# Kernel optimization log

Hardware: AMD Instinct MI355X
Metric: run time of the kernel (lower is better)

Reference implementation:

```python
import jax, jax.numpy as jnp
import numpy as np

KH = KW = 3
K = KH * KW
STRIDE = 1
PAD = 1
DIL = 1
GROUPS = 1
DG = 1  # deformable_groups
CIN = 256
COUT = 256
DC = 64  # depth_channels


def conv2d(x, w, b):
    out = jax.lax.conv_general_dilated(
        x, w, (STRIDE, STRIDE), [(PAD, PAD), (PAD, PAD)],
        rhs_dilation=(DIL, DIL), dimension_numbers=('NCHW', 'OIHW', 'NCHW'))
    return out + b[None, :, None, None]


def deform_sample(x, offset, mask):
    """Modulated deformable im2col. x:[N,C,H,W], offset:[N,DG*2*K,Ho,Wo],
    mask:[N,DG*K,Ho,Wo] or None. Returns cols [N,C,K,Ho,Wo]."""
    N, C, H, W = x.shape
    Ho = (H + 2 * PAD - (DIL * (KH - 1) + 1)) // STRIDE + 1
    Wo = (W + 2 * PAD - (DIL * (KW - 1) + 1)) // STRIDE + 1
    ky, kx = jnp.meshgrid(jnp.arange(KH), jnp.arange(KW), indexing='ij')
    # base sampling grid per kernel tap: [K,Ho,Wo]
    base_y = (jnp.arange(Ho) * STRIDE - PAD)[None, :, None] + (ky.reshape(-1) * DIL)[:, None, None]
    base_x = (jnp.arange(Wo) * STRIDE - PAD)[None, None, :] + (kx.reshape(-1) * DIL)[:, None, None]
    off = offset.reshape(N, DG, K, 2, Ho, Wo)  # [...,0]=dy, [...,1]=dx (CUDA layout)
    y = base_y[None, None].astype(x.dtype) + off[:, :, :, 0]
    xx = base_x[None, None].astype(x.dtype) + off[:, :, :, 1]
    y0 = jnp.floor(y)
    x0 = jnp.floor(xx)
    ly = y - y0
    lx = xx - x0
    y0i = y0.astype(jnp.int32)
    x0i = x0.astype(jnp.int32)
    xg = x.reshape(N, DG, C // DG, H * W)

    def gather(iy, ix):
        valid = ((iy >= 0) & (iy < H) & (ix >= 0) & (ix < W)).astype(x.dtype)
        idx = (jnp.clip(iy, 0, H - 1) * W + jnp.clip(ix, 0, W - 1)).reshape(N, DG, 1, K * Ho * Wo)
        v = jnp.take_along_axis(xg, idx, axis=3).reshape(N, DG, C // DG, K, Ho, Wo)
        return v * valid[:, :, None]

    v00 = gather(y0i, x0i)
    v01 = gather(y0i, x0i + 1)
    v10 = gather(y0i + 1, x0i)
    v11 = gather(y0i + 1, x0i + 1)
    w00 = (1 - ly) * (1 - lx)
    w01 = (1 - ly) * lx
    w10 = ly * (1 - lx)
    w11 = ly * lx
    cols = (v00 * w00[:, :, None] + v01 * w01[:, :, None]
            + v10 * w10[:, :, None] + v11 * w11[:, :, None])
    if mask is not None:
        cols = cols * mask.reshape(N, DG, 1, K, Ho, Wo)
    return cols.reshape(N, C, K, Ho, Wo)


def deform_conv2d(x, offset, mask, weight, bias):
    cols = deform_sample(x, offset, mask)  # [N,C,K,Ho,Wo]
    N, C, _, Ho, Wo = cols.shape
    Cout = weight.shape[0]
    cg = C // GROUPS
    cols = cols.reshape(N, GROUPS, cg * K, Ho * Wo)
    wg = weight.reshape(GROUPS, Cout // GROUPS, cg * K)
    out = jnp.einsum('gok,ngkp->ngop', wg, cols).reshape(N, Cout, Ho, Wo)
    return out + bias[None, :, None, None]


def setup_inputs() -> dict:
    key = jax.random.key(0)
    ks = jax.random.split(key, 8)
    x = jax.random.normal(ks[0], (4, CIN, 64, 64), dtype=jnp.float32)
    depth = jax.random.normal(ks[1], (4, DC, 64, 64), dtype=jnp.float32)
    stdv = 1.0 / np.sqrt(CIN * KH * KW)
    weight = jax.random.uniform(ks[2], (COUT, CIN // GROUPS, KH, KW), minval=-stdv, maxval=stdv, dtype=jnp.float32)
    bias = jnp.zeros((COUT,), jnp.float32)
    # offset/mask convs are zero-init in the module; use small random weights
    # so the irregular gather path is actually exercised.
    off_w = 0.05 * jax.random.normal(ks[3], (DG * 2 * K, CIN + DC, KH, KW), dtype=jnp.float32)
    off_b = 0.05 * jax.random.normal(ks[4], (DG * 2 * K,), dtype=jnp.float32)
    mask_w = 0.05 * jax.random.normal(ks[5], (DG * K, DC, KH, KW), dtype=jnp.float32)
    mask_b = 0.05 * jax.random.normal(ks[6], (DG * K,), dtype=jnp.float32)
    return {"x": x, "depth": depth, "weight": weight, "bias": bias,
            "off_w": off_w, "off_b": off_b, "mask_w": mask_w, "mask_b": mask_b}


def reference(x, depth, weight, bias, off_w, off_b, mask_w, mask_b):
    # offset = conv_offset(cat(x, depth))
    offset = conv2d(jnp.concatenate([x, depth], axis=1), off_w, off_b)
    # mask = sigmoid(DeformConv(depth, offset))  (non-modulated deform conv)
    mask = jax.nn.sigmoid(deform_conv2d(depth, offset, None, mask_w, mask_b))
    # modulated deformable conv on x
    return deform_conv2d(x, offset, mask, weight, bias)
```

## Files before the change

kernel.cpp:

```cpp
#include <hip/hip_runtime.h>


typedef __bf16 bf16x8 __attribute__((ext_vector_type(8)));
typedef float f32x4 __attribute__((ext_vector_type(4)));
typedef float float2_u __attribute__((ext_vector_type(2), aligned(4)));

__device__ __forceinline__ unsigned short f2bf(float f) {
  unsigned b = __float_as_uint(f);
  return (unsigned short)((b + 0x7fffu + ((b >> 16) & 1u)) >> 16);
}

__global__ __launch_bounds__(256) void k_prep_weight(
    const float* __restrict__ w, unsigned short* __restrict__ wbf)
{
  const int i = blockIdx.x * 256 + threadIdx.x;
  wbf[i] = f2bf(w[i]);
}

__global__ __launch_bounds__(256) void k_offset_conv(
    const float* __restrict__ x, const float* __restrict__ depth,
    const float* __restrict__ off_w, const float* __restrict__ off_b,
    float* __restrict__ offs)
{
  const int seg = blockIdx.x >> 8;
  const int nh  = blockIdx.x & 255;
  const int n = nh >> 6, ho = nh & 63;
  const int tid = threadIdx.x;
  const int lane = tid & 63;
  const int wave = tid >> 6;

  float acc[18];
#pragma unroll
  for (int i = 0; i < 18; ++i) acc[i] = 0.f;

  const int c0 = __builtin_amdgcn_readfirstlane(seg * 80 + wave * 20);

  for (int ci = 0; ci < 20; ++ci) {
    const int c = c0 + ci;
    const float* p = (c < 256) ? (x + (((n << 8) + c) << 12))
                               : (depth + (((n << 6) + (c - 256)) << 12));
    const float v0 = (ho > 0)  ? p[((ho - 1) << 6) + lane] : 0.f;
    const float v1 =             p[( ho      << 6) + lane];
    const float v2 = (ho < 63) ? p[((ho + 1) << 6) + lane] : 0.f;

    float v[9];
#pragma unroll
    for (int ky = 0; ky < 3; ++ky) {
      const float r = (ky == 0) ? v0 : ((ky == 1) ? v1 : v2);
#pragma unroll
      for (int kx = 0; kx < 3; ++kx) {
        const int src = lane + kx - 1;
        const float s = __shfl(r, src & 63);
        v[ky * 3 + kx] = (src >= 0 && src < 64) ? s : 0.f;
      }
    }
    const float* wp = off_w + c * 9;
#pragma unroll
    for (int co = 0; co < 18; ++co) {
      const float* w = wp + co * 2880;
#pragma unroll
      for (int t = 0; t < 9; ++t) acc[co] += v[t] * w[t];
    }
  }

  __shared__ float red[4][18][64];
#pragma unroll
  for (int co = 0; co < 18; ++co) red[wave][co][lane] = acc[co];
  __syncthreads();
  for (int o = tid; o < 18 * 64; o += 256) {
    const int co = o >> 6, wo = o & 63;
    float s = red[0][co][wo] + red[1][co][wo] + red[2][co][wo] + red[3][co][wo];
    if (seg == 0) s += off_b[co];
    atomicAdd(&offs[((n * 18 + co) << 12) + (ho << 6) + wo], s);
  }
}

__global__ __launch_bounds__(512) void k_mask_conv(
    const float* __restrict__ depth, const float* __restrict__ offs,
    const float* __restrict__ mask_w, const float* __restrict__ mask_b,
    float* __restrict__ mask)
{
  const int n  = blockIdx.x >> 6;
  const int ho = blockIdx.x & 63;
  const int tid  = threadIdx.x;
  const int lane = tid & 63;
  const int wave = tid >> 6;
  const int wo = lane;

  int i00[9], i01[9], i10[9], i11[9];
  float cw00[9], cw01[9], cw10[9], cw11[9];
  const float* op = offs + ((n * 18) << 12) + (ho << 6) + wo;
#pragma unroll
  for (int k = 0; k < 9; ++k) {
    const float dy = op[(2 * k) << 12];
    const float dx = op[(2 * k + 1) << 12];
    const float yy = (float)(ho - 1 + k / 3) + dy;
    const float xx = (float)(wo - 1 + k % 3) + dx;
    const float y0f = floorf(yy), x0f = floorf(xx);
    const float ly = yy - y0f, lx = xx - x0f;
    const int y0 = (int)y0f, x0 = (int)x0f;
    const int y0c = min(max(y0, 0), 63),     x0c = min(max(x0, 0), 63);
    const int y1c = min(max(y0 + 1, 0), 63), x1c = min(max(x0 + 1, 0), 63);
    const float fy0 = (y0 >= 0 && y0 < 64) ? 1.f : 0.f;
    const float fy1 = (y0 >= -1 && y0 < 63) ? 1.f : 0.f;
    const float fx0 = (x0 >= 0 && x0 < 64) ? 1.f : 0.f;
    const float fx1 = (x0 >= -1 && x0 < 63) ? 1.f : 0.f;
    i00[k] = (y0c << 6) + x0c;  i01[k] = (y0c << 6) + x1c;
    i10[k] = (y1c << 6) + x0c;  i11[k] = (y1c << 6) + x1c;
    cw00[k] = (1.f - ly) * (1.f - lx) * fy0 * fx0;
    cw01[k] = (1.f - ly) * lx * fy0 * fx1;
    cw10[k] = ly * (1.f - lx) * fy1 * fx0;
    cw11[k] = ly * lx * fy1 * fx1;
  }

  float acc[9];
#pragma unroll
  for (int i = 0; i < 9; ++i) acc[i] = 0.f;

  const int cbase = __builtin_amdgcn_readfirstlane(wave * 8);
  for (int cc = 0; cc < 8; ++cc) {
    const int c = cbase + cc;
    const float* p = depth + (((n << 6) + c) << 12);
    float val[9];
#pragma unroll
    for (int k = 0; k < 9; ++k) {
      val[k] = p[i00[k]] * cw00[k] + p[i01[k]] * cw01[k] +
               p[i10[k]] * cw10[k] + p[i11[k]] * cw11[k];
    }
    const float* wp = mask_w + c * 9;
#pragma unroll
    for (int co = 0; co < 9; ++co) {
#pragma unroll
      for (int k = 0; k < 9; ++k) acc[co] += val[k] * wp[co * 576 + k];
    }
  }

  __shared__ float red[8][9][64];
#pragma unroll
  for (int co = 0; co < 9; ++co) red[wave][co][lane] = acc[co];
  __syncthreads();
  for (int o = tid; o < 9 * 64; o += 512) {
    const int co = o >> 6, w2 = o & 63;
    float s = mask_b[co];
#pragma unroll
    for (int w = 0; w < 8; ++w) s += red[w][co][w2];
    mask[((n * 9 + co) << 12) + (ho << 6) + w2] = 1.f / (1.f + expf(-s));
  }
}

__device__ __forceinline__ void stage_channel8k(const float* src, float* dstb,
                                                int lane) {
  const char* s = (const char*)src + lane * 16;
  char* d = (char*)dstb;
#pragma unroll
  for (int j = 0; j < 8; ++j)
    __builtin_amdgcn_global_load_lds(
        (const __attribute__((address_space(1))) void*)(s + j * 1024),
        (__attribute__((address_space(3))) void*)(d + j * 1024), 16, 0, 0);
}

__global__ __launch_bounds__(512, 2) void k_deform_gemm(
    const float* __restrict__ x, const float* __restrict__ offs,
    const float* __restrict__ mask, const unsigned short* __restrict__ wbf,
    const float* __restrict__ bias, float* __restrict__ out)
{
  __shared__ float strip[9 * 2048];
  __shared__ __align__(16) unsigned short Bs[64][72];
  __shared__ float4 pwT[9][64];
  __shared__ int    piT[9][64];
  __shared__ int    piF[9][64];

  const int tid = threadIdx.x;
  const int b    = blockIdx.x;
  const int xcd  = b & 7, bslot = b >> 3;
  const int n    = xcd >> 1;
  const int ho   = ((xcd & 1) << 5) + bslot;
  const int pxb  = ho << 6;
  const int ylo  = min(max(ho - 15, 0), 32);

  for (int e = tid; e < 576; e += 512) {
    const int tap = e >> 6, pl = e & 63;
    const int wo = pl;
    const float dy = offs[((n * 18 + 2 * tap) << 12) + pxb + pl];
    const float dx = offs[((n * 18 + 2 * tap + 1) << 12) + pxb + pl];
    const float m  = mask[((n * 9 + tap) << 12) + pxb + pl];
    const float yy = (float)(ho - 1 + tap / 3) + dy;
    const float xx = (float)(wo - 1 + tap % 3) + dx;
    const float y0f = floorf(yy), x0f = floorf(xx);
    const float ly = yy - y0f, lx = xx - x0f;
    const int y0 = (int)y0f, x0 = (int)x0f;
    const int y0c = min(max(y0, 0), 63);
    const int y1c = min(max(y0 + 1, 0), 63);
    const float fy0 = (y0 >= 0 && y0 < 64) ? 1.f : 0.f;
    const float fy1 = (y0 >= -1 && y0 < 63) ? 1.f : 0.f;
    const int x0c = min(max(x0, 0), 63);
    const int x1c = min(max(x0 + 1, 0), 63);
    const int bx  = min(max(x0, 0), 62);
    const float vx0 = (x0 >= 0 && x0 < 64) ? 1.f : 0.f;
    const float vx1 = (x0 >= -1 && x0 < 63) ? 1.f : 0.f;
    const float wl = (1.f - lx) * vx0 * ((x0c == bx) ? 1.f : 0.f)
                   + lx * vx1 * ((x1c == bx) ? 1.f : 0.f);
    const float wr = (1.f - lx) * vx0 * ((x0c == bx + 1) ? 1.f : 0.f)
                   + lx * vx1 * ((x1c == bx + 1) ? 1.f : 0.f);
    const float a0 = (1.f - ly) * fy0 * m;
    const float a1 = ly * fy1 * m;
    pwT[tap][pl] = make_float4(wl * a0, wr * a0, wl * a1, wr * a1);
    const int ry0 = y0c - ylo, ry1 = y1c - ylo;
    const int ry0c = min(max(ry0, 0), 31), ry1c = min(max(ry1, 0), 31);
    const int bad = ((ry0 != ry0c) || (ry1 != ry1c)) ? 1 : 0;
    const int ad0 = (ry0c << 8) | (bx << 2);
    const int ad1 = (ry1c << 8) | (bx << 2);
    piT[tap][pl] = ad0 | (ad1 << 13) | (bad << 26);
    piF[tap][pl] = bx | (y0c << 6) | (y1c << 12);
  }

  const int pxl  = tid & 63;
  const int oct  = tid >> 6;
  const int lane = tid & 63;
  const int mrow = lane & 15;
  const int koct = lane >> 4;
  const float* xn = x + ((long)(n << 8) << 12);
  const char* xnc = (const char*)xn;
  const char* stripb = (const char*)strip;

  stage_channel8k(xn + (oct << 12) + (ylo << 6), &strip[oct * 2048], lane);
  int c_staged = 8;
  __syncthreads();

  auto gather = [&](int ic) {
    const int k0 = (ic << 6) + (oct << 3);
    int tp[8], sof[8];
#pragma unroll
    for (int j = 0; j < 8; ++j) {
      const int k = k0 + j;
      const int c = (int)(((unsigned)k * 7282u) >> 16);
      tp[j] = k - 9 * c;
      const int s9 = (int)(((unsigned)c * 7282u) >> 16);
      sof[j] = (c - 9 * s9) << 13;
    }
    int pk[8];
#pragma unroll
    for (int j = 0; j < 8; ++j) pk[j] = piT[tp[j]][pxl];
    float4 w[8];
#pragma unroll
    for (int j = 0; j < 8; ++j) w[j] = pwT[tp[j]][pxl];
    float2_u A[8], B[8];
#pragma unroll
    for (int j = 0; j < 8; ++j) {
      A[j] = *(const float2_u*)(stripb + sof[j] + (pk[j] & 8191));
      B[j] = *(const float2_u*)(stripb + sof[j] + ((pk[j] >> 13) & 8191));
    }
    int badm = 0;
    __align__(16) unsigned short v[8];
#pragma unroll
    for (int j = 0; j < 8; ++j) {
      v[j] = f2bf(A[j].x * w[j].x + A[j].y * w[j].y +
                  B[j].x * w[j].z + B[j].y * w[j].w);
      badm |= (pk[j] >> 26) << j;
    }
    if (__builtin_expect(badm != 0, 0)) {
#pragma unroll
      for (int j = 0; j < 8; ++j) if (badm & (1 << j)) {
        const int k = k0 + j;
        const int c = (int)(((unsigned)k * 7282u) >> 16);
        const char* pg = xnc + ((long)c << 14);
        const int pf = piF[tp[j]][pxl];
        const int bx = pf & 63, y0c = (pf >> 6) & 63, y1c = (pf >> 12) & 63;
        const float2_u Ag = *(const float2_u*)(pg + ((((y0c << 6) + bx)) << 2));
        const float2_u Bg = *(const float2_u*)(pg + ((((y1c << 6) + bx)) << 2));
        v[j] = f2bf(Ag.x * w[j].x + Ag.y * w[j].y +
                    Bg.x * w[j].z + Bg.y * w[j].w);
      }
    }
    *(int4*)&Bs[pxl][oct << 3] = *(const int4*)v;
  };

  bf16x8 afc[2][2];
#pragma unroll
  for (int mt = 0; mt < 2; ++mt)
#pragma unroll
    for (int ks = 0; ks < 2; ++ks) {
      const int row = (oct << 5) + (mt << 4) + mrow;
      const int col = (ks << 5) + (koct << 3);
      afc[mt][ks] = *(const bf16x8*)(wbf + row * 2304 + col);
    }

  gather(0);
  __syncthreads();

  f32x4 acc[2][4];
#pragma unroll
  for (int mt = 0; mt < 2; ++mt)
#pragma unroll
    for (int nt = 0; nt < 4; ++nt)
#pragma unroll
      for (int r = 0; r < 4; ++r) acc[mt][nt][r] = 0.f;

  for (int ic = 0; ic < 36; ++ic) {
    if (ic < 35) {
      const int c_end = (64 * ic + 127) / 9;
      const int cw = c_staged + oct;
      if (cw <= c_end) {
        const int slt = cw - 9 * (int)(((unsigned)cw * 7282u) >> 16);
        stage_channel8k(xn + (cw << 12) + (ylo << 6), &strip[slt * 2048], lane);
      }
      c_staged = c_end + 1;
    }

    bf16x8 afn[2][2];
    if (ic < 35) {
      const int kc = (ic + 1) << 6;
#pragma unroll
      for (int mt = 0; mt < 2; ++mt)
#pragma unroll
        for (int ks = 0; ks < 2; ++ks) {
          const int row = (oct << 5) + (mt << 4) + mrow;
          const int col = kc + (ks << 5) + (koct << 3);
          afn[mt][ks] = *(const bf16x8*)(wbf + row * 2304 + col);
        }
    }

#pragma unroll
    for (int ks = 0; ks < 2; ++ks)
#pragma unroll
      for (int nt = 0; nt < 4; ++nt) {
        const bf16x8 bfr =
            *(const bf16x8*)&Bs[(nt << 4) + mrow][(ks << 5) + (koct << 3)];
        acc[0][nt] = __builtin_amdgcn_mfma_f32_16x16x32_bf16(afc[0][ks], bfr,
                                                             acc[0][nt], 0, 0, 0);
        acc[1][nt] = __builtin_amdgcn_mfma_f32_16x16x32_bf16(afc[1][ks], bfr,
                                                             acc[1][nt], 0, 0, 0);
      }

    __syncthreads();
    if (ic < 35) gather(ic + 1);
    __syncthreads();

#pragma unroll
    for (int mt = 0; mt < 2; ++mt)
#pragma unroll
      for (int ks = 0; ks < 2; ++ks) afc[mt][ks] = afn[mt][ks];
  }

#pragma unroll
  for (int mt = 0; mt < 2; ++mt)
#pragma unroll
    for (int nt = 0; nt < 4; ++nt)
#pragma unroll
      for (int r = 0; r < 4; ++r) {
        const int co = (oct << 5) + (mt << 4) + ((lane >> 4) << 2) + r;
        const int pxg = pxb + (nt << 4) + (lane & 15);
        out[(((n << 8) + co) << 12) + pxg] = acc[mt][nt][r] + bias[co];
      }
}

extern "C" void kernel_launch(void* const* d_in, const int* in_sizes, int n_in,
                              void* d_out, int out_size, void* d_ws, size_t ws_size,
                              hipStream_t stream) {
  const float* x      = (const float*)d_in[0];
  const float* depth  = (const float*)d_in[1];
  const float* weight = (const float*)d_in[2];
  const float* bias   = (const float*)d_in[3];
  const float* off_w  = (const float*)d_in[4];
  const float* off_b  = (const float*)d_in[5];
  const float* mask_w = (const float*)d_in[6];
  const float* mask_b = (const float*)d_in[7];
  float* out = (float*)d_out;

  float* offs = (float*)d_ws;
  float* mask = offs + 294912;
  unsigned short* wbf = (unsigned short*)(mask + 147456);

  hipMemsetAsync(offs, 0, 294912 * sizeof(float), stream);
  k_prep_weight<<<2304, 256, 0, stream>>>(weight, wbf);
  k_offset_conv<<<1024, 256, 0, stream>>>(x, depth, off_w, off_b, offs);
  k_mask_conv<<<256, 512, 0, stream>>>(depth, offs, mask_w, mask_b, mask);
  k_deform_gemm<<<256, 512, 0, stream>>>(x, offs, mask, wbf, bias, out);
}
```

Measured before the change: 264.2 us.

## Keep sampling params in registers, pad LDS strip rows, stage via registers

Per-tap bilinear weights and packed addresses move from shared-memory tables into per-thread registers. The gather loop is specialised at compile time on the starting tap via a switch, and the strip base offsets become wave-uniform scalars. The input strip rows are padded to 272 bytes to cut LDS bank conflicts on the gather reads. Staging switches from global_load_lds to register loads written to LDS after the MFMA block. The rare out-of-strip fallback now recomputes its offsets from global memory, which costs more registers and risks lower occupancy.

```diff
diff --git a/kernel.cpp b/kernel.cpp
--- a/kernel.cpp
+++ b/kernel.cpp
@@ -4,6 +4,8 @@
 typedef __bf16 bf16x8 __attribute__((ext_vector_type(8)));
 typedef float f32x4 __attribute__((ext_vector_type(4)));
 typedef float float2_u __attribute__((ext_vector_type(2), aligned(4)));
+
+template <int N> struct IC { static constexpr int v = N; };
 
 __device__ __forceinline__ unsigned short f2bf(float f) {
   unsigned b = __float_as_uint(f);
@@ -148,27 +150,13 @@
   }
 }
 
-__device__ __forceinline__ void stage_channel8k(const float* src, float* dstb,
-                                                int lane) {
-  const char* s = (const char*)src + lane * 16;
-  char* d = (char*)dstb;
-#pragma unroll
-  for (int j = 0; j < 8; ++j)
-    __builtin_amdgcn_global_load_lds(
-        (const __attribute__((address_space(1))) void*)(s + j * 1024),
-        (__attribute__((address_space(3))) void*)(d + j * 1024), 16, 0, 0);
-}
-
 __global__ __launch_bounds__(512, 2) void k_deform_gemm(
     const float* __restrict__ x, const float* __restrict__ offs,
     const float* __restrict__ mask, const unsigned short* __restrict__ wbf,
     const float* __restrict__ bias, float* __restrict__ out)
 {
-  __shared__ float strip[9 * 2048];
+  __shared__ float strip[9 * 2176];
   __shared__ __align__(16) unsigned short Bs[64][72];
-  __shared__ float4 pwT[9][64];
-  __shared__ int    piT[9][64];
-  __shared__ int    piF[9][64];
 
   const int tid = threadIdx.x;
   const int b    = blockIdx.x;
@@ -178,12 +166,31 @@
   const int pxb  = ho << 6;
   const int ylo  = min(max(ho - 15, 0), 32);
 
-  for (int e = tid; e < 576; e += 512) {
-    const int tap = e >> 6, pl = e & 63;
-    const int wo = pl;
-    const float dy = offs[((n * 18 + 2 * tap) << 12) + pxb + pl];
-    const float dx = offs[((n * 18 + 2 * tap + 1) << 12) + pxb + pl];
-    const float m  = mask[((n * 9 + tap) << 12) + pxb + pl];
+  const int pxl  = tid & 63;
+  const int oct  = tid >> 6;
+  const int lane = tid & 63;
+  const int mrow = lane & 15;
+  const int koct = lane >> 4;
+  const float* xn = x + ((long)(n << 8) << 12);
+  const char* xnc = (const char*)xn;
+  const char* stripc = (const char*)strip;
+
+  float4 stg[8];
+  {
+    const char* src = (const char*)(xn + (oct << 12) + (ylo << 6)) + lane * 16;
+#pragma unroll
+    for (int i = 0; i < 8; ++i)
+      stg[i] = *(const float4*)(src + i * 1024);
+  }
+
+  float4 pw_[9];
+  int    pi_[9];
+#pragma unroll
+  for (int tap = 0; tap < 9; ++tap) {
+    const int wo = pxl;
+    const float dy = offs[((n * 18 + 2 * tap) << 12) + pxb + pxl];
+    const float dx = offs[((n * 18 + 2 * tap + 1) << 12) + pxb + pxl];
+    const float m  = mask[((n * 9 + tap) << 12) + pxb + pxl];
     const float yy = (float)(ho - 1 + tap / 3) + dy;
     const float xx = (float)(wo - 1 + tap % 3) + dx;
     const float y0f = floorf(yy), x0f = floorf(xx);
@@ -204,72 +211,93 @@
                    + lx * vx1 * ((x1c == bx + 1) ? 1.f : 0.f);
     const float a0 = (1.f - ly) * fy0 * m;
     const float a1 = ly * fy1 * m;
-    pwT[tap][pl] = make_float4(wl * a0, wr * a0, wl * a1, wr * a1);
+    pw_[tap] = make_float4(wl * a0, wr * a0, wl * a1, wr * a1);
     const int ry0 = y0c - ylo, ry1 = y1c - ylo;
     const int ry0c = min(max(ry0, 0), 31), ry1c = min(max(ry1, 0), 31);
     const int bad = ((ry0 != ry0c) || (ry1 != ry1c)) ? 1 : 0;
-    const int ad0 = (ry0c << 8) | (bx << 2);
-    const int ad1 = (ry1c << 8) | (bx << 2);
-    piT[tap][pl] = ad0 | (ad1 << 13) | (bad << 26);
-    piF[tap][pl] = bx | (y0c << 6) | (y1c << 12);
-  }
-
-  const int pxl  = tid & 63;
-  const int oct  = tid >> 6;
-  const int lane = tid & 63;
-  const int mrow = lane & 15;
-  const int koct = lane >> 4;
-  const float* xn = x + ((long)(n << 8) << 12);
-  const char* xnc = (const char*)xn;
-  const char* stripb = (const char*)strip;
-
-  stage_channel8k(xn + (oct << 12) + (ylo << 6), &strip[oct * 2048], lane);
+    const int ad0 = ry0c * 272 + (bx << 2);
+    const int ad1 = ry1c * 272 + (bx << 2);
+    pi_[tap] = ad0 | (ad1 << 14) | (bad << 28);
+  }
+
+  {
+    char* dst = (char*)strip + oct * 8704 + (lane >> 4) * 272 + (lane & 15) * 16;
+#pragma unroll
+    for (int i = 0; i < 8; ++i)
+      *(float4*)(dst + i * 4 * 272) = stg[i];
+  }
   int c_staged = 8;
   __syncthreads();
 
   auto gather = [&](int ic) {
     const int k0 = (ic << 6) + (oct << 3);
-    int tp[8], sof[8];
-#pragma unroll
-    for (int j = 0; j < 8; ++j) {
-      const int k = k0 + j;
-      const int c = (int)(((unsigned)k * 7282u) >> 16);
-      tp[j] = k - 9 * c;
-      const int s9 = (int)(((unsigned)c * 7282u) >> 16);
-      sof[j] = (c - 9 * s9) << 13;
-    }
-    int pk[8];
-#pragma unroll
-    for (int j = 0; j < 8; ++j) pk[j] = piT[tp[j]][pxl];
-    float4 w[8];
-#pragma unroll
-    for (int j = 0; j < 8; ++j) w[j] = pwT[tp[j]][pxl];
-    float2_u A[8], B[8];
-#pragma unroll
-    for (int j = 0; j < 8; ++j) {
-      A[j] = *(const float2_u*)(stripb + sof[j] + (pk[j] & 8191));
-      B[j] = *(const float2_u*)(stripb + sof[j] + ((pk[j] >> 13) & 8191));
-    }
-    int badm = 0;
+    const int c0 = (int)(((unsigned)k0 * 7282u) >> 16);
+    const int t0 = k0 - 9 * c0;
+    const int s9 = (int)(((unsigned)c0 * 7282u) >> 16);
+    const int s0 = c0 - 9 * s9;
+    const int sb0 = __builtin_amdgcn_readfirstlane(s0 * 8704);
+    const int sb1 = __builtin_amdgcn_readfirstlane(((s0 == 8) ? 0 : s0 + 1) * 8704);
+    const int t0s = __builtin_amdgcn_readfirstlane(t0);
+
     __align__(16) unsigned short v[8];
-#pragma unroll
-    for (int j = 0; j < 8; ++j) {
-      v[j] = f2bf(A[j].x * w[j].x + A[j].y * w[j].y +
-                  B[j].x * w[j].z + B[j].y * w[j].w);
-      badm |= (pk[j] >> 26) << j;
-    }
+    unsigned badm = 0;
+
+    auto body = [&](auto tc) {
+      constexpr int T0 = decltype(tc)::v;
+#pragma unroll
+      for (int j = 0; j < 8; ++j) {
+        const int tap = (T0 + j < 9) ? (T0 + j) : (T0 + j - 9);
+        const int sb  = (T0 + j < 9) ? sb0 : sb1;
+        const int pk  = pi_[tap];
+        const float4 w = pw_[tap];
+        const float2_u A = *(const float2_u*)(stripc + sb + (pk & 16383));
+        const float2_u B = *(const float2_u*)(stripc + sb + ((pk >> 14) & 16383));
+        v[j] = f2bf(A.x * w.x + A.y * w.y + B.x * w.z + B.y * w.w);
+        badm |= (((unsigned)pk >> 28) & 1u) << j;
+      }
+    };
+    switch (t0s) {
+      case 0: body(IC<0>{}); break;  case 1: body(IC<1>{}); break;
+      case 2: body(IC<2>{}); break;  case 3: body(IC<3>{}); break;
+      case 4: body(IC<4>{}); break;  case 5: body(IC<5>{}); break;
+      case 6: body(IC<6>{}); break;  case 7: body(IC<7>{}); break;
+      default: body(IC<8>{}); break;
+    }
+
     if (__builtin_expect(badm != 0, 0)) {
 #pragma unroll
-      for (int j = 0; j < 8; ++j) if (badm & (1 << j)) {
+      for (int j = 0; j < 8; ++j) if (badm & (1u << j)) {
         const int k = k0 + j;
         const int c = (int)(((unsigned)k * 7282u) >> 16);
+        const int tap = k - 9 * c;
+        const float dy = offs[((n * 18 + 2 * tap) << 12) + pxb + pxl];
+        const float dx = offs[((n * 18 + 2 * tap + 1) << 12) + pxb + pxl];
+        const float m  = mask[((n * 9 + tap) << 12) + pxb + pxl];
+        const float yy = (float)(ho - 1 + tap / 3) + dy;
+        const float xx = (float)(pxl - 1 + tap % 3) + dx;
+        const float y0f = floorf(yy), x0f = floorf(xx);
+        const float ly = yy - y0f, lx = xx - x0f;
+        const int y0 = (int)y0f, x0 = (int)x0f;
+        const int y0c = min(max(y0, 0), 63);
+        const int y1c = min(max(y0 + 1, 0), 63);
+        const float fy0 = (y0 >= 0 && y0 < 64) ? 1.f : 0.f;
+        const float fy1 = (y0 >= -1 && y0 < 63) ? 1.f : 0.f;
+        const int x0c = min(max(x0, 0), 63);
+        const int x1c = min(max(x0 + 1, 0), 63);
+        const int bx  = min(max(x0, 0), 62);
+        const float vx0 = (x0 >= 0 && x0 < 64) ? 1.f : 0.f;
+        const float vx1 = (x0 >= -1 && x0 < 63) ? 1.f : 0.f;
+        const float wl = (1.f - lx) * vx0 * ((x0c == bx) ? 1.f : 0.f)
+                       + lx * vx1 * ((x1c == bx) ? 1.f : 0.f);
+        const float wr = (1.f - lx) * vx0 * ((x0c == bx + 1) ? 1.f : 0.f)
+                       + lx * vx1 * ((x1c == bx + 1) ? 1.f : 0.f);
+        const float a0 = (1.f - ly) * fy0 * m;
+        const float a1 = ly * fy1 * m;
         const char* pg = xnc + ((long)c << 14);
-        const int pf = piF[tp[j]][pxl];
-        const int bx = pf & 63, y0c = (pf >> 6) & 63, y1c = (pf >> 12) & 63;
-        const float2_u Ag = *(const float2_u*)(pg + ((((y0c << 6) + bx)) << 2));
-        const float2_u Bg = *(const float2_u*)(pg + ((((y1c << 6) + bx)) << 2));
-        v[j] = f2bf(Ag.x * w[j].x + Ag.y * w[j].y +
-                    Bg.x * w[j].z + Bg.y * w[j].w);
+        const float2_u Ag = *(const float2_u*)(pg + (((y0c << 6) + bx) << 2));
+        const float2_u Bg = *(const float2_u*)(pg + (((y1c << 6) + bx) << 2));
+        v[j] = f2bf(Ag.x * (wl * a0) + Ag.y * (wr * a0) +
+                    Bg.x * (wl * a1) + Bg.y * (wr * a1));
       }
     }
     *(int4*)&Bs[pxl][oct << 3] = *(const int4*)v;
@@ -297,12 +325,18 @@
       for (int r = 0; r < 4; ++r) acc[mt][nt][r] = 0.f;
 
   for (int ic = 0; ic < 36; ++ic) {
+    bool do_stage = false;
+    int slt = 0;
     if (ic < 35) {
       const int c_end = (64 * ic + 127) / 9;
       const int cw = c_staged + oct;
-      if (cw <= c_end) {
-        const int slt = cw - 9 * (int)(((unsigned)cw * 7282u) >> 16);
-        stage_channel8k(xn + (cw << 12) + (ylo << 6), &strip[slt * 2048], lane);
+      do_stage = (cw <= c_end);
+      if (do_stage) {
+        slt = cw - 9 * (int)(((unsigned)cw * 7282u) >> 16);
+        const char* src = (const char*)(xn + (cw << 12) + (ylo << 6)) + lane * 16;
+#pragma unroll
+        for (int i = 0; i < 8; ++i)
+          stg[i] = *(const float4*)(src + i * 1024);
       }
       c_staged = c_end + 1;
     }
@@ -331,6 +365,13 @@
         acc[1][nt] = __builtin_amdgcn_mfma_f32_16x16x32_bf16(afc[1][ks], bfr,
                                                              acc[1][nt], 0, 0, 0);
       }
+
+    if (do_stage) {
+      char* dst = (char*)strip + slt * 8704 + (lane >> 4) * 272 + (lane & 15) * 16;
+#pragma unroll
+      for (int i = 0; i < 8; ++i)
+        *(float4*)(dst + i * 4 * 272) = stg[i];
+    }
 
     __syncthreads();
     if (ic < 35) gather(ic + 1);
```

Result: slower. 416.6 us (+57.7%).
